# Kernel tuning notes

Measured on AMD Instinct MI355X. Metric: run time of the kernel, lower is better.

Reference implementation:

```python
import jax, jax.numpy as jnp
import numpy as np

N, E, MUL, HID = 50000, 400000, 32, 64


def setup_inputs() -> dict:
    key = jax.random.key(0)
    ks = jax.random.split(key, 16)
    inp = {
        'node_scalars': jax.random.normal(ks[0], (N, MUL), jnp.float32),
        'node_vectors': jax.random.normal(ks[1], (N, MUL, 3), jnp.float32),
        'sh': jax.random.normal(ks[2], (E, 4), jnp.float32),
        'norm': jax.random.uniform(ks[3], (E, 1), jnp.float32),
        'mlp_w1': jax.random.normal(ks[4], (1, HID), jnp.float32),
        'mlp_b1': jnp.zeros((HID,), jnp.float32),
        'mlp_w2': jax.random.normal(ks[5], (HID, HID), jnp.float32) / np.sqrt(HID),
        'mlp_b2': jnp.zeros((HID,), jnp.float32),
        'mlp_w3': jax.random.normal(ks[6], (HID, 4 * MUL), jnp.float32) / np.sqrt(HID),
        'mlp_b3': jnp.zeros((4 * MUL,), jnp.float32),
        'lin1_w_s': jax.random.normal(ks[7], (2 * MUL, 6 * MUL), jnp.float32),
        'lin1_w_v': jax.random.normal(ks[8], (2 * MUL, 2 * MUL), jnp.float32),
        'lin2_w_s': jax.random.normal(ks[9], (5 * MUL, MUL), jnp.float32),
        'lin2_w_v': jax.random.normal(ks[10], (3 * MUL, MUL), jnp.float32),
        'senders': jax.random.randint(ks[11], (E,), 0, N, jnp.int32),
        'receivers': jax.random.randint(ks[12], (E,), 0, N, jnp.int32),
    }
    return inp


def reference(node_scalars, node_vectors, sh, norm,
              mlp_w1, mlp_b1, mlp_w2, mlp_b2, mlp_w3, mlp_b3,
              lin1_w_s, lin1_w_v, lin2_w_s, lin2_w_v,
              senders, receivers):
    n = node_scalars.shape[0]
    y0, y1 = sh[:, :1], sh[:, 1:]                      # 0e SH [E,1], 1o SH [E,3]
    # ---- gather sender features ----
    s_e = node_scalars[senders]                         # [E,MUL]
    v_e = node_vectors[senders]                         # [E,MUL,3]
    # ---- CG tensor product (sh 0e+1o) x (MULx0e + MULx1o) -> 2MULx0e + 2MULx1o ----
    tp_s = jnp.concatenate([y0 * s_e,
                            jnp.einsum('ek,emk->em', y1, v_e) / jnp.sqrt(3.0)], axis=-1)   # [E,2MUL]
    tp_v = jnp.concatenate([y0[:, :, None] * v_e,
                            y1[:, None, :] * s_e[:, :, None]], axis=1)                      # [E,2MUL,3]
    # ---- MLP on edge norms -> one gating scalar per output irrep (4MUL) ----
    h = jax.nn.silu(norm @ mlp_w1 + mlp_b1)
    h = jax.nn.silu(h @ mlp_w2 + mlp_b2)
    scal = h @ mlp_w3 + mlp_b3                          # [E,4MUL]
    m2 = tp_s.shape[-1]
    tp_s = tp_s * scal[:, :m2]
    tp_v = tp_v * scal[:, m2:, None]
    # ---- scatter-mean into receivers ----
    cnt = jax.ops.segment_sum(jnp.ones((receivers.shape[0],), tp_s.dtype), receivers, num_segments=n)
    denom = jnp.maximum(cnt, 1.0)[:, None]
    agg_s = jax.ops.segment_sum(tp_s, receivers, num_segments=n) / denom                    # [N,2MUL]
    agg_v = jax.ops.segment_sum(tp_v, receivers, num_segments=n) / denom[:, :, None]        # [N,2MUL,3]
    # ---- equivariant Linear -> irreps + gate scalars ----
    x_s = agg_s @ lin1_w_s / jnp.sqrt(jnp.float32(agg_s.shape[-1]))                         # [N,6MUL]
    x_v = jnp.einsum('nmi,mo->noi', agg_v, lin1_w_v) / jnp.sqrt(jnp.float32(agg_v.shape[1]))# [N,2MUL,3]
    n_vec = x_v.shape[1]
    act_s = jax.nn.silu(x_s[:, : x_s.shape[-1] - n_vec])                                    # [N,4MUL]
    gates = jax.nn.sigmoid(x_s[:, x_s.shape[-1] - n_vec:])                                  # [N,2MUL]
    g_v = x_v * gates[:, :, None]
    # ---- concat skip + final Linear to output irreps (MULx0e + MULx1o) ----
    c_s = jnp.concatenate([act_s, node_scalars], axis=-1)                                   # [N,5MUL]
    c_v = jnp.concatenate([g_v, node_vectors], axis=1)                                      # [N,3MUL,3]
    o_s = c_s @ lin2_w_s / jnp.sqrt(jnp.float32(c_s.shape[-1]))                             # [N,MUL]
    o_v = jnp.einsum('nmi,mo->noi', c_v, lin2_w_v) / jnp.sqrt(jnp.float32(c_v.shape[1]))    # [N,MUL,3]
    return jnp.concatenate([o_s, o_v.reshape(o_v.shape[0], -1)], axis=-1)                   # [N,4MUL]
```

## Files before the change

kernel.cpp:

```cpp
#include <hip/hip_runtime.h>

#define NN 50000
#define NE 400000
#define NBINS 1024
#define NSBIN 512

#define RL1ST 0
#define RL1VT 12288
#define RL2S  16384
#define RL2V  21504
#define WTOT  24576

#define SLUT_N ((NBINS+1)*256)
#define INTS_N (3*NN + 1 + NE + 1024)
#define FIXED_FL ((size_t)WTOT + SLUT_N + INTS_N)

#define SCAN_B 196

#define S160 0.07905694150420949f
#define S96  0.10206207261596576f

__device__ __forceinline__ float sigf(float x){
  return __builtin_amdgcn_rcpf(1.0f + __expf(-x));
}
__device__ __forceinline__ float siluf(float x){ return x * sigf(x); }

__global__ __launch_bounds__(256) void convert_weights(
    const float* __restrict__ l1s, const float* __restrict__ l1v,
    const float* __restrict__ l2s, const float* __restrict__ l2v,
    float* __restrict__ wgt)
{
  int i = blockIdx.x*256 + threadIdx.x;
  if (i < 12288){ int o=i>>6, m=i&63; wgt[RL1ST + i] = l1s[m*192+o]; return; }
  if (i < 16384){ int t=i-12288; int o=t>>6, m=t&63; wgt[RL1VT + t] = l1v[m*64+o]; return; }
  if (i < 21504){ int t=i-16384; wgt[RL2S + t] = l2s[t]; return; }
  if (i < 24576){ int t=i-21504; wgt[RL2V + t] = l2v[t]; return; }
}

__global__ __launch_bounds__(128) void build_lut(
    const float* __restrict__ w1, const float* __restrict__ b1,
    const float* __restrict__ w2, const float* __restrict__ b2,
    const float* __restrict__ w3, const float* __restrict__ b3,
    float* __restrict__ slut)
{
  __shared__ float h1[64], h2[64], scal[128];
  int bin = blockIdx.x;
  float x = (float)bin / (float)NBINS;
  int t = threadIdx.x;
  if (t < 64) h1[t] = siluf(fmaf(x, w1[t], b1[t]));
  __syncthreads();
  if (t < 64){
    float a = b2[t];
    for (int k=0;k<64;k++) a = fmaf(h1[k], w2[k*64+t], a);
    h2[t] = siluf(a);
  }
  __syncthreads();
  {
    float a = b3[t];
    for (int k=0;k<64;k++) a = fmaf(h2[k], w3[k*128+t], a);
    scal[t] = a;
  }
  __syncthreads();
  for (int c=t; c<256; c+=128){
    int m=c>>3, q=c&7;
    int idx = (q==0)? m : (q==1)? (32+m) : (q<5)? (64+m) : (96+m);
    slut[(size_t)bin*256 + c] = scal[idx];
  }
}

__global__ __launch_bounds__(256) void count_kernel(
    const int* __restrict__ rcv, int* __restrict__ cnt)
{
  int e = blockIdx.x*256 + threadIdx.x;
  if (e < NE) atomicAdd(&cnt[rcv[e]], 1);
}

__global__ __launch_bounds__(256) void scan_a(
    const int* __restrict__ cnt, int* __restrict__ offs, int* __restrict__ bsum)
{
  __shared__ int sd[256];
  int tid = threadIdx.x;
  int i = blockIdx.x*256 + tid;
  int c = (i < NN) ? cnt[i] : 0;
  sd[tid] = c;
  __syncthreads();
  for (int off=1; off<256; off<<=1){
    int t = (tid >= off) ? sd[tid-off] : 0;
    __syncthreads();
    sd[tid] += t;
    __syncthreads();
  }
  if (i < NN) offs[i] = sd[tid] - c;
  if (tid == 255) bsum[blockIdx.x] = sd[255];
}

__global__ __launch_bounds__(256) void scan_b(
    const int* __restrict__ bsum, int* __restrict__ bbase, int* __restrict__ offs)
{
  __shared__ int sd[256];
  int tid = threadIdx.x;
  int v = (tid < SCAN_B) ? bsum[tid] : 0;
  sd[tid] = v;
  __syncthreads();
  for (int off=1; off<256; off<<=1){
    int t = (tid >= off) ? sd[tid-off] : 0;
    __syncthreads();
    sd[tid] += t;
    __syncthreads();
  }
  if (tid < SCAN_B) bbase[tid] = sd[tid] - v;
  if (tid == 255) offs[NN] = sd[255];
}

__global__ __launch_bounds__(256) void scan_c(
    const int* __restrict__ bbase, int* __restrict__ offs, int* __restrict__ curs)
{
  int i = blockIdx.x*256 + threadIdx.x;
  if (i < NN){
    int o = offs[i] + bbase[blockIdx.x];
    offs[i] = o;
    curs[i] = o;
  }
}

__global__ __launch_bounds__(256) void scatter_kernel(
    const int* __restrict__ rcv, int* __restrict__ curs, int* __restrict__ eids)
{
  int e = blockIdx.x*256 + threadIdx.x;
  if (e >= NE) return;
  int pos = atomicAdd(&curs[rcv[e]], 1);
  eids[pos] = e;
}

__global__ __launch_bounds__(256) void dhist_kernel(
    const int* __restrict__ offs, int* __restrict__ hist, int cn0, int cnn)
{
  __shared__ int lh[NSBIN];
  for (int j=threadIdx.x; j<NSBIN; j+=256) lh[j]=0;
  __syncthreads();
  int i = blockIdx.x*256 + threadIdx.x;
  if (i < cnn){
    int n = cn0 + i;
    int d = offs[n+1] - offs[n];
    int b = (d < NSBIN) ? (NSBIN-1-d) : 0;
    atomicAdd(&lh[b], 1);
  }
  __syncthreads();
  for (int j=threadIdx.x; j<NSBIN; j+=256){
    int v = lh[j];
    if (v) atomicAdd(&hist[j], v);
  }
}

__global__ __launch_bounds__(512) void dhist_scan(int* __restrict__ hist)
{
  __shared__ int sd[512];
  int t = threadIdx.x;
  int v = hist[t];
  sd[t] = v;
  __syncthreads();
  for (int off=1; off<512; off<<=1){
    int x = (t >= off) ? sd[t-off] : 0;
    __syncthreads();
    sd[t] += x;
    __syncthreads();
  }
  hist[t] = sd[t] - v;
}

__global__ __launch_bounds__(256) void dsort_kernel(
    const int* __restrict__ offs, int* __restrict__ hist,
    int* __restrict__ sorted, int cn0, int cnn)
{
  __shared__ int lh[NSBIN];
  __shared__ int lb[NSBIN];
  for (int j=threadIdx.x; j<NSBIN; j+=256) lh[j]=0;
  __syncthreads();
  int i = blockIdx.x*256 + threadIdx.x;
  int b = -1, rank = 0;
  if (i < cnn){
    int n = cn0 + i;
    int d = offs[n+1] - offs[n];
    b = (d < NSBIN) ? (NSBIN-1-d) : 0;
    rank = atomicAdd(&lh[b], 1);
  }
  __syncthreads();
  for (int j=threadIdx.x; j<NSBIN; j+=256){
    int v = lh[j];
    lb[j] = v ? atomicAdd(&hist[j], v) : 0;
  }
  __syncthreads();
  if (i < cnn) sorted[cn0 + lb[b] + rank] = cn0 + i;
}

__global__ __launch_bounds__(256) void edge_agg_kernel(
    const float* __restrict__ ns, const float* __restrict__ nv,
    const float* __restrict__ sh, const float* __restrict__ nrm,
    const int* __restrict__ snd,
    const int* __restrict__ offs, const int* __restrict__ eids,
    const int* __restrict__ sorted,
    const float* __restrict__ slut,
    float* __restrict__ agg, int cn0, int cnn)
{
  int wave = threadIdx.x >> 6;
  int lane = threadIdx.x & 63;
  int nls = blockIdx.x*4 + wave;
  if (nls >= cnn) return;
  int n = sorted[cn0 + nls];
  int m = lane >> 1;
  int odd = lane & 1;
  int p0 = offs[n], p1 = offs[n+1];
  const float4* slut4 = (const float4*)slut;
  const float inv_sqrt3 = 0.57735026918962576f;
  float a0=0.f, a1=0.f, a2=0.f, a3=0.f;

  if (p0 < p1){
    const int plast = p1 - 1;

#define LDM(P, S, X, Y) { int _e = eids[(P)]; S = snd[_e]; X = nrm[_e]; \
                          Y = *(const float4*)(sh + 4*_e); }
#define GLOAD(S, X, Y, Gtt, GLa, GLb, Gse, Gw, Gv2, Gy) { \
    float _f = fminf(fmaxf((X)*(float)NBINS, 0.0f), (float)NBINS - 0.001f); \
    int _b = (int)_f; Gtt = _f - (float)_b; \
    GLa = slut4[(size_t)_b*64 + lane]; \
    GLb = slut4[(size_t)(_b+1)*64 + lane]; \
    Gse = ns[(size_t)(S)*32 + m]; \
    Gw  = *(const float2*)(nv + (size_t)(S)*96 + 3*m); \
    Gv2 = nv[(size_t)(S)*96 + 3*m + 2]; \
    Gy = Y; }

    int sA, sB, sC;  float xA, xB, xC;  float4 yA, yB, yC;
    LDM(p0, sA, xA, yA);
    { int pm = (p0+1 <= plast) ? (p0+1) : plast; LDM(pm, sB, xB, yB); }
    { int pm = (p0+2 <= plast) ? (p0+2) : plast; LDM(pm, sC, xC, yC); }

    float tt0; float4 La0, Lb0; float se0; float2 w0; float vv0; float4 y0;
    float tt1; float4 La1, Lb1; float se1; float2 w1; float vv1; float4 y1;
    GLOAD(sA, xA, yA, tt0, La0, Lb0, se0, w0, vv0, y0);
    GLOAD(sB, xB, yB, tt1, La1, Lb1, se1, w1, vv1, y1);

    for (int p = p0; p <= plast; ++p){
      int sD; float xD; float4 yD;
      { int pm = (p+3 <= plast) ? (p+3) : plast; LDM(pm, sD, xD, yD); }
      float tt2; float4 La2, Lb2; float se2; float2 w2; float vv2; float4 y2;
      GLOAD(sC, xC, yC, tt2, La2, Lb2, se2, w2, vv2, y2);

      float sc0 = fmaf(tt0, Lb0.x-La0.x, La0.x);
      float sc1 = fmaf(tt0, Lb0.y-La0.y, La0.y);
      float sc2 = fmaf(tt0, Lb0.z-La0.z, La0.z);
      float sc3 = fmaf(tt0, Lb0.w-La0.w, La0.w);
      float A0,A1,A2,A3;
      if (!odd){
        float dot = fmaf(y0.w, vv0, fmaf(y0.z, w0.y, y0.y*w0.x));
        A0 = y0.x*se0; A1 = dot*inv_sqrt3; A2 = y0.x*w0.x; A3 = y0.x*w0.y;
      } else {
        A0 = y0.x*vv0; A1 = y0.y*se0; A2 = y0.z*se0; A3 = y0.w*se0;
      }
      a0 = fmaf(A0, sc0, a0);
      a1 = fmaf(A1, sc1, a1);
      a2 = fmaf(A2, sc2, a2);
      a3 = fmaf(A3, sc3, a3);

      tt0=tt1; La0=La1; Lb0=Lb1; se0=se1; w0=w1; vv0=vv1; y0=y1;
      tt1=tt2; La1=La2; Lb1=Lb2; se1=se2; w1=w2; vv1=vv2; y1=y2;
      sC=sD; xC=xD; yC=yD;
    }
#undef LDM
#undef GLOAD
  }
  int deg = p1 - p0;
  float inv = (deg > 0) ? __builtin_amdgcn_rcpf((float)deg) : 1.0f;
  float* ap = agg + (size_t)(n - cn0)*256;
  int pos0 = odd ? (192+m) : m;
  int pos1 = odd ? ( 96+m) : (32+m);
  int pos2 = odd ? (160+m) : (64+m);
  int pos3 = odd ? (224+m) : (128+m);
  ap[pos0] = a0*inv;
  ap[pos1] = a1*inv;
  ap[pos2] = a2*inv;
  ap[pos3] = a3*inv;
}

__global__ __launch_bounds__(256) __attribute__((amdgpu_waves_per_eu(3,8)))
void node_s_kernel(
    const float* __restrict__ ns, const float* __restrict__ wgt,
    const float* __restrict__ agg, int cn0, int cnn,
    float* __restrict__ out)
{
  __shared__ float red[3*64*33];
  int lane = threadIdx.x & 63, role = threadIdx.x >> 6;
  int ro = __builtin_amdgcn_readfirstlane(role);
  int nl = blockIdx.x*64 + lane;
  bool valid = (nl < cnn);
  int nls = valid ? nl : (cnn-1);
  int n = cn0 + nl;

  float aggs[64];
  float oacc[32];
  #pragma unroll
  for (int j=0;j<32;j++) oacc[j]=0.0f;

  {
    const float4* ar = (const float4*)(agg + (size_t)nls*256);
    #pragma unroll
    for (int g=0; g<16; g++){
      float4 v = ar[g];
      aggs[4*g+0]=v.x; aggs[4*g+1]=v.y; aggs[4*g+2]=v.z; aggs[4*g+3]=v.w;
    }
  }
  const float* l1sT = wgt + RL1ST + ro*32*64;
  const float* l2s  = wgt + RL2S;
  for (int t=0;t<32;t++){
    const float4* col = (const float4*)(l1sT + t*64);
    float d0=0,d1=0,d2=0,d3=0;
    #pragma unroll
    for (int j=0;j<16;j++){
      float4 c = col[j];
      d0 = fmaf(aggs[4*j+0], c.x, d0);
      d1 = fmaf(aggs[4*j+1], c.y, d1);
      d2 = fmaf(aggs[4*j+2], c.z, d2);
      d3 = fmaf(aggs[4*j+3], c.w, d3);
    }
    float act = siluf(((d0+d1)+(d2+d3))*0.125f);
    const float4* row = (const float4*)(l2s + (size_t)(ro*32 + t)*32);
    #pragma unroll
    for (int j=0;j<8;j++){
      float4 w = row[j];
      oacc[4*j+0] = fmaf(act, w.x, oacc[4*j+0]);
      oacc[4*j+1] = fmaf(act, w.y, oacc[4*j+1]);
      oacc[4*j+2] = fmaf(act, w.z, oacc[4*j+2]);
      oacc[4*j+3] = fmaf(act, w.w, oacc[4*j+3]);
    }
  }
  {
    const float4* sp = (const float4*)(ns + (size_t)(cn0+nls)*32 + ro*8);
    #pragma unroll
    for (int q4=0;q4<2;q4++){
      float4 v = sp[q4];
      float vv[4] = {v.x, v.y, v.z, v.w};
      #pragma unroll
      for (int u=0;u<4;u++){
        int q = ro*8 + q4*4 + u;
        const float4* row = (const float4*)(l2s + (size_t)(128+q)*32);
        #pragma unroll
        for (int j=0;j<8;j++){
          float4 w = row[j];
          oacc[4*j+0] = fmaf(vv[u], w.x, oacc[4*j+0]);
          oacc[4*j+1] = fmaf(vv[u], w.y, oacc[4*j+1]);
          oacc[4*j+2] = fmaf(vv[u], w.z, oacc[4*j+2]);
          oacc[4*j+3] = fmaf(vv[u], w.w, oacc[4*j+3]);
        }
      }
    }
  }

  if (role != 0){
    float* rp = red + (role-1)*(64*33) + lane*33;
    #pragma unroll
    for (int j=0;j<32;j++) rp[j] = oacc[j];
  }
  __syncthreads();
  if (role == 0 && valid){
    #pragma unroll
    for (int j=0;j<32;j++)
      oacc[j] += red[0*(64*33)+lane*33+j] + red[1*(64*33)+lane*33+j]
               + red[2*(64*33)+lane*33+j];
    float4* op = (float4*)(out + (size_t)n*128);
    #pragma unroll
    for (int j=0;j<8;j++){
      float4 o4;
      o4.x = oacc[4*j+0]*S160; o4.y = oacc[4*j+1]*S160;
      o4.z = oacc[4*j+2]*S160; o4.w = oacc[4*j+3]*S160;
      op[j] = o4;
    }
  }
}

__global__ __launch_bounds__(192) __attribute__((amdgpu_waves_per_eu(3,8)))
void node_v_kernel(
    const float* __restrict__ nv, const float* __restrict__ wgt,
    const float* __restrict__ agg, int cn0, int cnn,
    float* __restrict__ out)
{
  __shared__ float sw[64*97];
  int lane = threadIdx.x & 63, role = threadIdx.x >> 6;
  int ro = __builtin_amdgcn_readfirstlane(role);
  int nl = blockIdx.x*64 + lane;
  bool valid = (nl < cnn);
  int nls = valid ? nl : (cnn-1);
  const float* arow = agg + (size_t)nls*256;

  {
    float aggs[64];
    const float4* ar = (const float4*)arow;
    #pragma unroll
    for (int g=0; g<16; g++){
      float4 v = ar[g];
      aggs[4*g+0]=v.x; aggs[4*g+1]=v.y; aggs[4*g+2]=v.z; aggs[4*g+3]=v.w;
    }
    const float* l1g = wgt + RL1ST + 128*64;
    for (int o=ro; o<64; o+=3){
      const float4* col = (const float4*)(l1g + o*64);
      float d0=0,d1=0,d2=0,d3=0;
      #pragma unroll
      for (int j=0;j<16;j++){
        float4 c = col[j];
        d0 = fmaf(aggs[4*j+0], c.x, d0);
        d1 = fmaf(aggs[4*j+1], c.y, d1);
        d2 = fmaf(aggs[4*j+2], c.z, d2);
        d3 = fmaf(aggs[4*j+3], c.w, d3);
      }
      sw[o*64+lane] = sigf(((d0+d1)+(d2+d3))*0.125f);
    }
  }
  __syncthreads();

  int k = role;
  float aggv[64], oacc[32];
  #pragma unroll
  for (int j=0;j<32;j++) oacc[j]=0.0f;
  {
    const float4* av = (const float4*)(arow + 64 + 64*k);
    #pragma unroll
    for (int g=0; g<16; g++){
      float4 v = av[g];
      aggv[4*g+0]=v.x; aggv[4*g+1]=v.y; aggv[4*g+2]=v.z; aggv[4*g+3]=v.w;
    }
  }
  const float* l1vT = wgt + RL1VT;
  const float* l2v  = wgt + RL2V;
  for (int o=0;o<64;o++){
    const float4* col = (const float4*)(l1vT + o*64);
    float d0=0,d1=0,d2=0,d3=0;
    #pragma unroll
    for (int j=0;j<16;j++){
      float4 c = col[j];
      d0 = fmaf(aggv[4*j+0], c.x, d0);
      d1 = fmaf(aggv[4*j+1], c.y, d1);
      d2 = fmaf(aggv[4*j+2], c.z, d2);
      d3 = fmaf(aggv[4*j+3], c.w, d3);
    }
    float gv = (((d0+d1)+(d2+d3))*0.125f) * sw[o*64+lane];
    const float4* row = (const float4*)(l2v + (size_t)o*32);
    #pragma unroll
    for (int j=0;j<8;j++){
      float4 w = row[j];
      oacc[4*j+0] = fmaf(gv, w.x, oacc[4*j+0]);
      oacc[4*j+1] = fmaf(gv, w.y, oacc[4*j+1]);
      oacc[4*j+2] = fmaf(gv, w.z, oacc[4*j+2]);
      oacc[4*j+3] = fmaf(gv, w.w, oacc[4*j+3]);
    }
  }
  {
    const float* vp = nv + (size_t)(cn0+nls)*96 + k;
    #pragma unroll 8
    for (int q=0;q<32;q++){
      float a = vp[3*q];
      const float4* row = (const float4*)(l2v + (size_t)(64+q)*32);
      #pragma unroll
      for (int j=0;j<8;j++){
        float4 w = row[j];
        oacc[4*j+0] = fmaf(a, w.x, oacc[4*j+0]);
        oacc[4*j+1] = fmaf(a, w.y, oacc[4*j+1]);
        oacc[4*j+2] = fmaf(a, w.z, oacc[4*j+2]);
        oacc[4*j+3] = fmaf(a, w.w, oacc[4*j+3]);
      }
    }
  }

  __syncthreads();
  if (valid){
    #pragma unroll
    for (int j=0;j<32;j++) sw[lane*97 + 3*j + k] = oacc[j]*S96;
  }
  __syncthreads();
  int nb = blockIdx.x*64;
  #pragma unroll
  for (int r=0;r<8;r++){
    int F = r*192 + threadIdx.x;
    int i = F/24, j = F%24;
    if (nb + i < cnn){
      float4 o4;
      o4.x = sw[i*97 + 4*j + 0];
      o4.y = sw[i*97 + 4*j + 1];
      o4.z = sw[i*97 + 4*j + 2];
      o4.w = sw[i*97 + 4*j + 3];
      *(float4*)(out + (size_t)(cn0+nb+i)*128 + 32 + 4*j) = o4;
    }
  }
}

extern "C" void kernel_launch(void* const* d_in, const int* in_sizes, int n_in,
                              void* d_out, int out_size, void* d_ws, size_t ws_size,
                              hipStream_t stream) {
  const float* node_scalars = (const float*)d_in[0];
  const float* node_vectors = (const float*)d_in[1];
  const float* sh           = (const float*)d_in[2];
  const float* norm         = (const float*)d_in[3];
  const float* w1  = (const float*)d_in[4];
  const float* b1  = (const float*)d_in[5];
  const float* w2  = (const float*)d_in[6];
  const float* b2  = (const float*)d_in[7];
  const float* w3  = (const float*)d_in[8];
  const float* b3  = (const float*)d_in[9];
  const float* l1s = (const float*)d_in[10];
  const float* l1v = (const float*)d_in[11];
  const float* l2s = (const float*)d_in[12];
  const float* l2v = (const float*)d_in[13];
  const int* snd = (const int*)d_in[14];
  const int* rcv = (const int*)d_in[15];
  float* ws = (float*)d_ws;
  float* out = (float*)d_out;

  size_t ws_fl = ws_size / 4;
  if (ws_fl < FIXED_FL + 64*256) return;
  size_t aggcap = (ws_fl - FIXED_FL) / 256;
  int csize = (int)((aggcap < (size_t)NN) ? aggcap : (size_t)NN);
  int nchunks = (NN + csize - 1) / csize;

  float* wgt  = ws;
  float* slut = wgt + WTOT;
  int*   ib   = (int*)(slut + SLUT_N);
  int* offs   = ib;
  int* curs   = ib + NN + 1;
  int* eids   = ib + 2*NN + 1;
  int* sorted = ib + 2*NN + 1 + NE;
  int* cnt    = sorted;
  int* hist   = ib + 3*NN + 1 + NE;
  int* bsum   = hist + 512;
  int* bbase  = bsum + 256;
  float* agg  = (float*)(bbase + 256);

  hipMemsetAsync(cnt, 0, NN*sizeof(int), stream);

  convert_weights<<<(WTOT+255)/256, 256, 0, stream>>>(l1s, l1v, l2s, l2v, wgt);
  build_lut<<<NBINS+1, 128, 0, stream>>>(w1,b1,w2,b2,w3,b3, slut);

  count_kernel<<<(NE+255)/256, 256, 0, stream>>>(rcv, cnt);
  scan_a<<<SCAN_B, 256, 0, stream>>>(cnt, offs, bsum);
  scan_b<<<1, 256, 0, stream>>>(bsum, bbase, offs);
  scan_c<<<SCAN_B, 256, 0, stream>>>(bbase, offs, curs);
  scatter_kernel<<<(NE+255)/256, 256, 0, stream>>>(rcv, curs, eids);

  for (int ch = 0; ch < nchunks; ch++){
    int cn0 = ch * csize;
    int cnn = (NN - cn0 < csize) ? (NN - cn0) : csize;
    hipMemsetAsync(hist, 0, NSBIN*sizeof(int), stream);
    dhist_kernel<<<(cnn+255)/256, 256, 0, stream>>>(offs, hist, cn0, cnn);
    dhist_scan<<<1, 512, 0, stream>>>(hist);
    dsort_kernel<<<(cnn+255)/256, 256, 0, stream>>>(offs, hist, sorted, cn0, cnn);

    edge_agg_kernel<<<(cnn+3)/4, 256, 0, stream>>>(
        node_scalars, node_vectors, sh, norm, snd, offs, eids, sorted, slut,
        agg, cn0, cnn);
    node_s_kernel<<<(cnn+63)/64, 256, 0, stream>>>(
        node_scalars, wgt, agg, cn0, cnn, out);
    node_v_kernel<<<(cnn+63)/64, 192, 0, stream>>>(
        node_vectors, wgt, agg, cn0, cnn, out);
  }
}
```

Baseline: 382.7 us.

## Process two edges per wave with half-wave per edge and fold sqrt3 into LUT

Restructures the edge aggregation kernel so each wave handles two edges at once: each half-wave of 32 lanes takes one edge, with one lane per multiplicity channel computing all eight outputs, and the halves are combined with a cross-half shuffle at the end. The manual three-deep software prefetch pipeline is dropped in favour of a simple loop that masks the out-of-range edge. The 1/sqrt(3) factor is folded into the gating LUT at build time. The aim is to halve the per-node serial loop length and remove the odd/even lane divergence. The cost is more registers per lane, wasted work on odd-degree nodes, and losing the explicit latency hiding.

New measurement: 354.2 us. 1.08x faster.

```diff
diff --git a/kernel.cpp b/kernel.cpp
--- a/kernel.cpp
+++ b/kernel.cpp
@@ -64,7 +64,9 @@
   for (int c=t; c<256; c+=128){
     int m=c>>3, q=c&7;
     int idx = (q==0)? m : (q==1)? (32+m) : (q<5)? (64+m) : (96+m);
-    slut[(size_t)bin*256 + c] = scal[idx];
+    float v = scal[idx];
+    if (q == 1) v *= 0.57735026918962576f;
+    slut[(size_t)bin*256 + c] = v;
   }
 }
 
@@ -204,81 +206,77 @@
 {
   int wave = threadIdx.x >> 6;
   int lane = threadIdx.x & 63;
+  int es = lane >> 5;
+  int l  = lane & 31;
   int nls = blockIdx.x*4 + wave;
   if (nls >= cnn) return;
   int n = sorted[cn0 + nls];
-  int m = lane >> 1;
-  int odd = lane & 1;
   int p0 = offs[n], p1 = offs[n+1];
   const float4* slut4 = (const float4*)slut;
-  const float inv_sqrt3 = 0.57735026918962576f;
-  float a0=0.f, a1=0.f, a2=0.f, a3=0.f;
-
-  if (p0 < p1){
-    const int plast = p1 - 1;
-
-#define LDM(P, S, X, Y) { int _e = eids[(P)]; S = snd[_e]; X = nrm[_e]; \
-                          Y = *(const float4*)(sh + 4*_e); }
-#define GLOAD(S, X, Y, Gtt, GLa, GLb, Gse, Gw, Gv2, Gy) { \
-    float _f = fminf(fmaxf((X)*(float)NBINS, 0.0f), (float)NBINS - 0.001f); \
-    int _b = (int)_f; Gtt = _f - (float)_b; \
-    GLa = slut4[(size_t)_b*64 + lane]; \
-    GLb = slut4[(size_t)(_b+1)*64 + lane]; \
-    Gse = ns[(size_t)(S)*32 + m]; \
-    Gw  = *(const float2*)(nv + (size_t)(S)*96 + 3*m); \
-    Gv2 = nv[(size_t)(S)*96 + 3*m + 2]; \
-    Gy = Y; }
-
-    int sA, sB, sC;  float xA, xB, xC;  float4 yA, yB, yC;
-    LDM(p0, sA, xA, yA);
-    { int pm = (p0+1 <= plast) ? (p0+1) : plast; LDM(pm, sB, xB, yB); }
-    { int pm = (p0+2 <= plast) ? (p0+2) : plast; LDM(pm, sC, xC, yC); }
-
-    float tt0; float4 La0, Lb0; float se0; float2 w0; float vv0; float4 y0;
-    float tt1; float4 La1, Lb1; float se1; float2 w1; float vv1; float4 y1;
-    GLOAD(sA, xA, yA, tt0, La0, Lb0, se0, w0, vv0, y0);
-    GLOAD(sB, xB, yB, tt1, La1, Lb1, se1, w1, vv1, y1);
-
-    for (int p = p0; p <= plast; ++p){
-      int sD; float xD; float4 yD;
-      { int pm = (p+3 <= plast) ? (p+3) : plast; LDM(pm, sD, xD, yD); }
-      float tt2; float4 La2, Lb2; float se2; float2 w2; float vv2; float4 y2;
-      GLOAD(sC, xC, yC, tt2, La2, Lb2, se2, w2, vv2, y2);
-
-      float sc0 = fmaf(tt0, Lb0.x-La0.x, La0.x);
-      float sc1 = fmaf(tt0, Lb0.y-La0.y, La0.y);
-      float sc2 = fmaf(tt0, Lb0.z-La0.z, La0.z);
-      float sc3 = fmaf(tt0, Lb0.w-La0.w, La0.w);
-      float A0,A1,A2,A3;
-      if (!odd){
-        float dot = fmaf(y0.w, vv0, fmaf(y0.z, w0.y, y0.y*w0.x));
-        A0 = y0.x*se0; A1 = dot*inv_sqrt3; A2 = y0.x*w0.x; A3 = y0.x*w0.y;
-      } else {
-        A0 = y0.x*vv0; A1 = y0.y*se0; A2 = y0.z*se0; A3 = y0.w*se0;
-      }
-      a0 = fmaf(A0, sc0, a0);
-      a1 = fmaf(A1, sc1, a1);
-      a2 = fmaf(A2, sc2, a2);
-      a3 = fmaf(A3, sc3, a3);
-
-      tt0=tt1; La0=La1; Lb0=Lb1; se0=se1; w0=w1; vv0=vv1; y0=y1;
-      tt1=tt2; La1=La2; Lb1=Lb2; se1=se2; w1=w2; vv1=vv2; y1=y2;
-      sC=sD; xC=xD; yC=yD;
-    }
-#undef LDM
-#undef GLOAD
-  }
-  int deg = p1 - p0;
-  float inv = (deg > 0) ? __builtin_amdgcn_rcpf((float)deg) : 1.0f;
-  float* ap = agg + (size_t)(n - cn0)*256;
-  int pos0 = odd ? (192+m) : m;
-  int pos1 = odd ? ( 96+m) : (32+m);
-  int pos2 = odd ? (160+m) : (64+m);
-  int pos3 = odd ? (224+m) : (128+m);
-  ap[pos0] = a0*inv;
-  ap[pos1] = a1*inv;
-  ap[pos2] = a2*inv;
-  ap[pos3] = a3*inv;
+  float a0=0.f,a1=0.f,a2=0.f,a3=0.f,a4=0.f,a5=0.f,a6=0.f,a7=0.f;
+
+  for (int base = p0; base < p1; base += 2){
+    int p  = base + es;
+    int pc = (p < p1) ? p : (p1 - 1);
+    float ok = (p < p1) ? 1.0f : 0.0f;
+    int e = eids[pc];
+    int s = snd[e];
+    float x = nrm[e];
+    float4 y = *(const float4*)(sh + 4*e);
+
+    float f = fminf(fmaxf(x*(float)NBINS, 0.0f), (float)NBINS - 0.001f);
+    int b = (int)f;
+    float tt = f - (float)b;
+    const float4* Sp = slut4 + (size_t)b*64 + 2*l;
+    float4 La = Sp[0];
+    float4 Lb = Sp[1];
+    float4 Lc = Sp[64];
+    float4 Ld = Sp[65];
+
+    float se = ns[(size_t)s*32 + l] * ok;
+    const float* vp = nv + (size_t)s*96 + 3*l;
+    float2 w = *(const float2*)vp;
+    float v2 = vp[2];
+    float v0 = w.x*ok, v1 = w.y*ok; v2 *= ok;
+
+    float sc0 = fmaf(tt, Lc.x-La.x, La.x);
+    float sc1 = fmaf(tt, Lc.y-La.y, La.y);
+    float sc2 = fmaf(tt, Lc.z-La.z, La.z);
+    float sc3 = fmaf(tt, Lc.w-La.w, La.w);
+    float sc4 = fmaf(tt, Ld.x-Lb.x, Lb.x);
+    float sc5 = fmaf(tt, Ld.y-Lb.y, Lb.y);
+    float sc6 = fmaf(tt, Ld.z-Lb.z, Lb.z);
+    float sc7 = fmaf(tt, Ld.w-Lb.w, Lb.w);
+
+    float dot = fmaf(y.w, v2, fmaf(y.z, v1, y.y*v0));
+    a0 = fmaf(y.x*se, sc0, a0);
+    a1 = fmaf(dot,    sc1, a1);
+    a2 = fmaf(y.x*v0, sc2, a2);
+    a3 = fmaf(y.x*v1, sc3, a3);
+    a4 = fmaf(y.x*v2, sc4, a4);
+    a5 = fmaf(y.y*se, sc5, a5);
+    a6 = fmaf(y.z*se, sc6, a6);
+    a7 = fmaf(y.w*se, sc7, a7);
+  }
+
+  a0 += __shfl_xor(a0, 32); a1 += __shfl_xor(a1, 32);
+  a2 += __shfl_xor(a2, 32); a3 += __shfl_xor(a3, 32);
+  a4 += __shfl_xor(a4, 32); a5 += __shfl_xor(a5, 32);
+  a6 += __shfl_xor(a6, 32); a7 += __shfl_xor(a7, 32);
+
+  if (es == 0){
+    int deg = p1 - p0;
+    float inv = (deg > 0) ? __builtin_amdgcn_rcpf((float)deg) : 1.0f;
+    float* ap = agg + (size_t)(n - cn0)*256;
+    ap[l]       = a0*inv;
+    ap[32+l]    = a1*inv;
+    ap[64+l]    = a2*inv;
+    ap[128+l]   = a3*inv;
+    ap[192+l]   = a4*inv;
+    ap[96+l]    = a5*inv;
+    ap[160+l]   = a6*inv;
+    ap[224+l]   = a7*inv;
+  }
 }
 
 __global__ __launch_bounds__(256) __attribute__((amdgpu_waves_per_eu(3,8)))
```
